# Kernel optimization log

Measured on AMD Instinct MI355X. Metric: run time of the kernel, lower is better.

The kernel has to match this reference:

```python
import jax, jax.numpy as jnp
import numpy as np

B, S, D_MODEL = 2, 2048, 1024
H, D = 16, 64
D_INNER = H * D
EPS = 1e-5


def setup_inputs() -> dict:
    key = jax.random.key(0)
    ks = jax.random.split(key, 10)
    sc = 0.02
    return {
        "x": jax.random.normal(ks[0], (B, S, D_MODEL), dtype=jnp.float32),
        "Wq": jax.random.normal(ks[1], (D_MODEL, D_INNER), dtype=jnp.float32) * sc,
        "Wk": jax.random.normal(ks[2], (D_MODEL, D_INNER), dtype=jnp.float32) * sc,
        "Wv": jax.random.normal(ks[3], (D_MODEL, D_INNER), dtype=jnp.float32) * sc,
        "Wg": jax.random.normal(ks[4], (D_MODEL, D_INNER), dtype=jnp.float32) * sc,
        "Wa": jax.random.normal(ks[5], (D_MODEL, H), dtype=jnp.float32) * sc,
        "ba": jax.random.normal(ks[6], (H,), dtype=jnp.float32) * sc,
        "Wo": jax.random.normal(ks[7], (D_INNER, D_MODEL), dtype=jnp.float32) * sc,
        "gn_w": jnp.ones((D_INNER,), dtype=jnp.float32),
        "gn_b": jnp.zeros((D_INNER,), dtype=jnp.float32),
    }


def reference(x, Wq, Wk, Wv, Wg, Wa, ba, Wo, gn_w, gn_b):
    b, s, _ = x.shape
    # projections -> [B,H,S,D]
    q = jax.nn.silu(jnp.einsum('bsm,md->bsd', x, Wq).reshape(b, s, H, D).transpose(0, 2, 1, 3))
    k = jax.nn.silu(jnp.einsum('bsm,md->bsd', x, Wk).reshape(b, s, H, D).transpose(0, 2, 1, 3))
    v = jnp.einsum('bsm,md->bsd', x, Wv).reshape(b, s, H, D).transpose(0, 2, 1, 3)

    # data-dependent log forget gate, per head: [B,H,S]
    log_alpha = -jax.nn.softplus(jnp.einsum('bsm,mh->bsh', x, Wa) + ba)
    cum = jnp.cumsum(log_alpha, axis=1).transpose(0, 2, 1)  # [B,H,S]

    # decay[b,h,i,j] = exp(cum[i] - cum[j]) for j <= i, else 0
    diff = cum[:, :, :, None] - cum[:, :, None, :]  # [B,H,S,S]
    causal = jnp.tril(jnp.ones((s, s), dtype=bool))
    decay = jnp.exp(jnp.where(causal, diff, -jnp.inf))

    attn = jnp.einsum('bhid,bhjd->bhij', q, k) * decay
    o = jnp.einsum('bhij,bhjd->bhid', attn, v)  # [B,H,S,D]
    o = o.transpose(0, 2, 1, 3)  # [B,S,H,D]

    # GroupNorm(H groups) over channels-within-group and spatial dim S
    mean = jnp.mean(o, axis=(1, 3), keepdims=True)          # per (b,h)
    var = jnp.var(o, axis=(1, 3), keepdims=True)
    o = (o - mean) / jnp.sqrt(var + EPS)
    o = o * gn_w.reshape(H, D) + gn_b.reshape(H, D)
    o = o.reshape(b, s, H * D)

    gate = jax.nn.sigmoid(jnp.einsum('bsm,md->bsd', x, Wg))
    return jnp.einsum('bsd,dm->bsm', o * gate, Wo)
```

## Files before the change

kernel.cpp:

```cpp
#include <hip/hip_runtime.h>
#include <math.h>
#include <stdint.h>

typedef __attribute__((ext_vector_type(4))) float f32x4;
typedef __attribute__((ext_vector_type(8))) short bf16x8;

constexpr int NB = 2;
constexpr int NS = 2048;
constexpr int NM = 1024;
constexpr int NH = 16;
constexpr int ND = 64;
constexpr int NDI = 1024;

__device__ __forceinline__ float bf2f(unsigned short u) {
  uint32_t x = ((uint32_t)u) << 16; float f; __builtin_memcpy(&f, &x, 4); return f;
}
__device__ __forceinline__ unsigned short f2bf(float f) {
  uint32_t x; __builtin_memcpy(&x, &f, 4);
  x += 0x7FFFu + ((x >> 16) & 1u);
  return (unsigned short)(x >> 16);
}

__global__ __launch_bounds__(256) void k_prep(const float* __restrict__ x,
    const float* __restrict__ w0, const float* __restrict__ w1,
    const float* __restrict__ w2, const float* __restrict__ w3,
    const float* __restrict__ w4, const float* __restrict__ Wa,
    unsigned short* __restrict__ xb,
    unsigned short* __restrict__ t0, unsigned short* __restrict__ t1,
    unsigned short* __restrict__ t2, unsigned short* __restrict__ t3,
    unsigned short* __restrict__ t4, unsigned short* __restrict__ wa_pad) {
  int bid = blockIdx.x;
  if (bid < 2048) {
    int i = bid * 256 + threadIdx.x;
    const float4* p = (const float4*)(x + (size_t)i * 8);
    float4 a = p[0], b = p[1];
    unsigned short r[8] = {f2bf(a.x), f2bf(a.y), f2bf(a.z), f2bf(a.w),
                           f2bf(b.x), f2bf(b.y), f2bf(b.z), f2bf(b.w)};
    *(uint4*)(xb + (size_t)i * 8) = *(const uint4*)r;
  } else if (bid < 7168) {
    __shared__ float tile[32][33];
    int w = bid - 2048;
    int z = w >> 10, within = w & 1023;
    const float* src = z == 0 ? w0 : z == 1 ? w1 : z == 2 ? w2 : z == 3 ? w3 : w4;
    unsigned short* dst = z == 0 ? t0 : z == 1 ? t1 : z == 2 ? t2 : z == 3 ? t3 : t4;
    int c0 = (within & 31) * 32, r0 = (within >> 5) * 32;
    int tx = threadIdx.x & 31, ty = threadIdx.x >> 5;
    #pragma unroll
    for (int i = 0; i < 4; i++)
      tile[ty + i * 8][tx] = src[(size_t)(r0 + ty + i * 8) * 1024 + c0 + tx];
    __syncthreads();
    #pragma unroll
    for (int i = 0; i < 4; i++)
      dst[(size_t)(c0 + ty + i * 8) * 1024 + r0 + tx] = f2bf(tile[tx][ty + i * 8]);
  } else {
    int idx = (bid - 7168) * 256 + threadIdx.x;
    int h = idx >> 10, k2 = idx & 1023;
    wa_pad[idx] = (h < 16) ? f2bf(Wa[k2 * 16 + h]) : (unsigned short)0;
  }
}

__global__ __launch_bounds__(256) void k_la_gemm(const unsigned short* __restrict__ xb,
    const unsigned short* __restrict__ wa_pad, float* __restrict__ la8) {
  __shared__ unsigned short As[128 * 32];
  __shared__ unsigned short Bs[128 * 32];
  int tid = threadIdx.x;
  int row0 = blockIdx.y * 128;
  int kbeg = blockIdx.x * 128;
  float* Cp = la8 + (size_t)blockIdx.x * (32 * 2048);
  int w = tid >> 6, l = tid & 63;
  int wr = w >> 1, wc = w & 1;
  int lr = l & 15, lk = l >> 4;
  f32x4 acc[4] = {};
  for (int k0 = kbeg; k0 < kbeg + 128; k0 += 32) {
    __syncthreads();
    #pragma unroll
    for (int i = 0; i < 2; i++) {
      int idx = tid + i * 256;
      int r = idx >> 2, c = idx & 3;
      int cs = c ^ ((r >> 1) & 3);
      const unsigned short* srcA = xb + (size_t)(row0 + r) * NM + k0 + cs * 8;
      const unsigned short* srcB = wa_pad + (size_t)r * NM + k0 + cs * 8;
      __builtin_amdgcn_global_load_lds(
          (const __attribute__((address_space(1))) void*)srcA,
          (__attribute__((address_space(3))) void*)((char*)As + (w * 64 + i * 256) * 16),
          16, 0, 0);
      __builtin_amdgcn_global_load_lds(
          (const __attribute__((address_space(1))) void*)srcB,
          (__attribute__((address_space(3))) void*)((char*)Bs + (w * 64 + i * 256) * 16),
          16, 0, 0);
    }
    __syncthreads();
    if (wc == 0) {
      bf16x8 b = *(const bf16x8*)&Bs[lr * 32 + (lk ^ ((lr >> 1) & 3)) * 8];
      #pragma unroll
      for (int m = 0; m < 4; m++) {
        int ra = wr * 64 + m * 16 + lr;
        bf16x8 a = *(const bf16x8*)&As[ra * 32 + (lk ^ ((ra >> 1) & 3)) * 8];
        acc[m] = __builtin_amdgcn_mfma_f32_16x16x32_bf16(a, b, acc[m], 0, 0, 0);
      }
    }
  }
  if (wc == 0) {
    #pragma unroll
    for (int m = 0; m < 4; m++) {
      #pragma unroll
      for (int j = 0; j < 4; j++) {
        int row = row0 + wr * 64 + m * 16 + lk * 4 + j;
        int bb = row >> 11, s = row & 2047;
        Cp[((size_t)(bb * 16 + lr)) * 2048 + s] = acc[m][j];
      }
    }
  }
}

__global__ __launch_bounds__(256) void k_cumsum(const float* __restrict__ la8,
    const float* __restrict__ ba, float* __restrict__ cum,
    float* __restrict__ psum, float* __restrict__ psq) {
  int g = blockIdx.x;
  int h = g & 15;
  if (threadIdx.x == 0) { psum[g] = 0.f; psq[g] = 0.f; }
  float bah = ba[h];
  const float* p0 = la8 + (size_t)g * NS;
  float* out = cum + (size_t)g * NS;
  __shared__ float part[256];
  float v[8]; float sum = 0.f;
  int base = threadIdx.x * 8;
  #pragma unroll
  for (int i = 0; i < 8; i++) {
    int s = base + i;
    float z = bah;
    #pragma unroll
    for (int sl = 0; sl < 8; sl++) z += p0[sl * 65536 + s];
    float sp = fmaxf(z, 0.f) + log1pf(expf(-fabsf(z)));
    v[i] = -sp; sum += v[i];
  }
  part[threadIdx.x] = sum;
  __syncthreads();
  for (int off = 1; off < 256; off <<= 1) {
    float add = (threadIdx.x >= off) ? part[threadIdx.x - off] : 0.f;
    __syncthreads();
    part[threadIdx.x] += add;
    __syncthreads();
  }
  float run = (threadIdx.x > 0) ? part[threadIdx.x - 1] : 0.f;
  #pragma unroll
  for (int i = 0; i < 8; i++) { run += v[i]; out[base + i] = run; }
}

__global__ __launch_bounds__(512, 2) void k_proj8(
    const unsigned short* __restrict__ A,
    const unsigned short* __restrict__ Wcat,
    unsigned short* __restrict__ q, unsigned short* __restrict__ k,
    unsigned short* __restrict__ v, unsigned short* __restrict__ g) {
  __shared__ unsigned short Ab[2][256 * 64];
  __shared__ unsigned short Bb[2][256 * 64];
  int tid = threadIdx.x;
  int bid = blockIdx.x;
  int wg = (bid & 7) * 32 + (bid >> 3);
  int bx = wg & 15, by = wg >> 4;
  int row0 = by * 256, col0 = bx * 256;
  int wid = tid >> 6, lane = tid & 63;
  int WR = wid >> 2, WC = wid & 3;
  int lr = lane & 15, lk = lane >> 4;

  auto stage = [&](int kt, int bi) {
    #pragma unroll
    for (int i = 0; i < 4; i++) {
      int idx = tid + i * 512;
      int r = idx >> 3, c = idx & 7;
      int cs = c ^ (r & 7);
      const unsigned short* srcA = A + (size_t)(row0 + r) * NM + kt * 64 + cs * 8;
      __builtin_amdgcn_global_load_lds(
          (const __attribute__((address_space(1))) void*)srcA,
          (__attribute__((address_space(3))) void*)((char*)&Ab[bi][0] + (wid * 64 + i * 512) * 16),
          16, 0, 0);
      const unsigned short* srcB = Wcat + (size_t)(col0 + r) * NM + kt * 64 + cs * 8;
      __builtin_amdgcn_global_load_lds(
          (const __attribute__((address_space(1))) void*)srcB,
          (__attribute__((address_space(3))) void*)((char*)&Bb[bi][0] + (wid * 64 + i * 512) * 16),
          16, 0, 0);
    }
  };

  stage(0, 0);
  stage(1, 1);

  f32x4 acc[8][4] = {};
  for (int kt = 0; kt < 16; ++kt) {
    int bi = kt & 1;
    if (kt < 15) asm volatile("s_waitcnt vmcnt(8)" ::: "memory");
    else         asm volatile("s_waitcnt vmcnt(0)" ::: "memory");
    __builtin_amdgcn_sched_barrier(0);
    __builtin_amdgcn_s_barrier();

    const char* Ap = (const char*)&Ab[bi][0];
    const char* Bp = (const char*)&Bb[bi][0];
    bf16x8 a0[8], b0[4], a1[8], b1[4];
    #pragma unroll
    for (int m = 0; m < 8; m++) {
      int r = WR * 128 + m * 16 + lr;
      a0[m] = *(const bf16x8*)(Ap + r * 128 + ((lk ^ (r & 7)) * 16));
    }
    #pragma unroll
    for (int n = 0; n < 4; n++) {
      int r = WC * 64 + n * 16 + lr;
      b0[n] = *(const bf16x8*)(Bp + r * 128 + ((lk ^ (r & 7)) * 16));
    }
    #pragma unroll
    for (int m = 0; m < 8; m++)
      #pragma unroll
      for (int n = 0; n < 4; n++)
        acc[m][n] = __builtin_amdgcn_mfma_f32_16x16x32_bf16(a0[m], b0[n], acc[m][n], 0, 0, 0);
    #pragma unroll
    for (int m = 0; m < 8; m++) {
      int r = WR * 128 + m * 16 + lr;
      a1[m] = *(const bf16x8*)(Ap + r * 128 + (((lk + 4) ^ (r & 7)) * 16));
    }
    #pragma unroll
    for (int n = 0; n < 4; n++) {
      int r = WC * 64 + n * 16 + lr;
      b1[n] = *(const bf16x8*)(Bp + r * 128 + (((lk + 4) ^ (r & 7)) * 16));
    }
    asm volatile("s_waitcnt lgkmcnt(0)" ::: "memory");
    __builtin_amdgcn_sched_barrier(0);
    __builtin_amdgcn_s_barrier();
    if (kt + 2 < 16) stage(kt + 2, bi);
    __builtin_amdgcn_s_setprio(1);
    #pragma unroll
    for (int m = 0; m < 8; m++)
      #pragma unroll
      for (int n = 0; n < 4; n++)
        acc[m][n] = __builtin_amdgcn_mfma_f32_16x16x32_bf16(a1[m], b1[n], acc[m][n], 0, 0, 0);
    __builtin_amdgcn_s_setprio(0);
  }

  #pragma unroll
  for (int m = 0; m < 8; m++) {
    #pragma unroll
    for (int n = 0; n < 4; n++) {
      int col = col0 + WC * 64 + n * 16 + lr;
      int zone = col >> 10;
      unsigned short* dst = zone == 0 ? q : zone == 1 ? k : zone == 2 ? v : g;
      int cb = col & 1023;
      #pragma unroll
      for (int j = 0; j < 4; j++) {
        int row = row0 + WR * 128 + m * 16 + lk * 4 + j;
        float val = acc[m][n][j];
        if (zone <= 1) val = val / (1.f + expf(-val));
        else if (zone == 3) val = 1.f / (1.f + expf(-val));
        dst[(size_t)row * 1024 + cb] = f2bf(val);
      }
    }
  }
}

__global__ __launch_bounds__(256) void k_out2(const unsigned short* __restrict__ A,
    const unsigned short* __restrict__ Bt, float* __restrict__ C) {
  __shared__ unsigned short As[2][128 * 64];
  __shared__ unsigned short Bs[2][128 * 64];
  int tid = threadIdx.x;
  int bid = blockIdx.x;
  int wg = (bid & 7) * 32 + (bid >> 3);
  int bx = wg & 7, by = wg >> 3;
  int row0 = by * 128, col0 = bx * 128;
  int w = tid >> 6, l = tid & 63;
  int wr = w >> 1, wc = w & 1;
  int lr = l & 15, lk = l >> 4;

  auto stage = [&](int t, int bi) {
    #pragma unroll
    for (int i = 0; i < 4; i++) {
      int idx = tid + i * 256;
      int r = idx >> 3, c = idx & 7;
      int cs = c ^ (r & 7);
      const unsigned short* srcA = A + (size_t)(row0 + r) * NM + t * 64 + cs * 8;
      __builtin_amdgcn_global_load_lds(
          (const __attribute__((address_space(1))) void*)srcA,
          (__attribute__((address_space(3))) void*)((char*)&As[bi][0] + idx * 16),
          16, 0, 0);
      const unsigned short* srcB = Bt + (size_t)(col0 + r) * NM + t * 64 + cs * 8;
      __builtin_amdgcn_global_load_lds(
          (const __attribute__((address_space(1))) void*)srcB,
          (__attribute__((address_space(3))) void*)((char*)&Bs[bi][0] + idx * 16),
          16, 0, 0);
    }
  };

  stage(0, 0);
  asm volatile("s_waitcnt vmcnt(0)" ::: "memory");
  __builtin_amdgcn_s_barrier();

  f32x4 acc[4][4] = {};
  int cur = 0;
  for (int t = 0; t < 16; ++t) {
    if (t < 15) stage(t + 1, cur ^ 1);
    const char* Ap = (const char*)&As[cur][0];
    const char* Bp = (const char*)&Bs[cur][0];
    bf16x8 a[4][2], b[4][2];
    #pragma unroll
    for (int m = 0; m < 4; m++) {
      int ra = wr * 64 + m * 16 + lr;
      #pragma unroll
      for (int kk = 0; kk < 2; kk++)
        a[m][kk] = *(const bf16x8*)(Ap + ra * 128 + (((kk * 4 + lk) ^ (ra & 7)) * 16));
    }
    #pragma unroll
    for (int n = 0; n < 4; n++) {
      int rb = wc * 64 + n * 16 + lr;
      #pragma unroll
      for (int kk = 0; kk < 2; kk++)
        b[n][kk] = *(const bf16x8*)(Bp + rb * 128 + (((kk * 4 + lk) ^ (rb & 7)) * 16));
    }
    __builtin_amdgcn_s_setprio(1);
    #pragma unroll
    for (int kk = 0; kk < 2; kk++)
      #pragma unroll
      for (int m = 0; m < 4; m++)
        #pragma unroll
        for (int n = 0; n < 4; n++)
          acc[m][n] = __builtin_amdgcn_mfma_f32_16x16x32_bf16(a[m][kk], b[n][kk], acc[m][n], 0, 0, 0);
    __builtin_amdgcn_s_setprio(0);
    asm volatile("s_waitcnt vmcnt(0)" ::: "memory");
    __builtin_amdgcn_s_barrier();
    cur ^= 1;
  }
  #pragma unroll
  for (int m = 0; m < 4; m++)
    #pragma unroll
    for (int n = 0; n < 4; n++)
      #pragma unroll
      for (int j = 0; j < 4; j++) {
        int row = row0 + wr * 64 + m * 16 + lk * 4 + j;
        int col = col0 + wc * 64 + n * 16 + lr;
        C[(size_t)row * NM + col] = acc[m][n][j];
      }
}

__global__ __launch_bounds__(256) void k_attn(const unsigned short* __restrict__ q,
    const unsigned short* __restrict__ kk, const unsigned short* __restrict__ vv,
    const float* __restrict__ cum, unsigned short* __restrict__ o,
    float* __restrict__ psum, float* __restrict__ psq) {
  int it = blockIdx.x, h = blockIdx.y, b = blockIdx.z;
  int i0 = it * 64;
  __shared__ unsigned short Qs[64 * 64];
  __shared__ unsigned short Ks[64 * 64];
  __shared__ unsigned short Ps[64 * 64];
  __shared__ unsigned short Vt[64 * 66];
  __shared__ float ci[64], cj[64];
  __shared__ int jlo_s;
  int tid = threadIdx.x;
  int w = tid >> 6, lane = tid & 63;
  int cl = lane & 15, hi = lane >> 4;
  const size_t hb = (size_t)b * NS * NDI + (size_t)h * ND;
  const float* cumh = cum + (size_t)(b * NH + h) * NS;

  #pragma unroll
  for (int lp = 0; lp < 2; lp++) {
    int idx = tid + lp * 256;
    int r = idx >> 3, cb = (idx & 7) * 16;
    uint4 t = *(const uint4*)(q + hb + (size_t)(i0 + r) * NDI + (cb >> 1));
    *(uint4*)((char*)Qs + r * 128 + (cb ^ ((r & 7) << 4))) = t;
  }
  if (tid < 64) ci[tid] = cumh[i0 + tid];
  if (tid < 64) {
    int jt = tid;
    bool ok = (jt <= it) && (cumh[i0] - cumh[jt * 64 + 63] >= -25.f);
    unsigned long long mask = __ballot(ok);
    if (tid == 0) jlo_s = (int)__builtin_ctzll(mask);
  }
  __syncthreads();
  int jlo = jlo_s;

  int arow = w * 16 + cl;
  int xr = (cl & 7) << 4;
  const char* Qb = (const char*)Qs + arow * 128;
  const char* Pb = (const char*)Ps + arow * 128;
  f32x4 acco[4] = {};

  for (int jt = jlo; jt <= it; jt++) {
    int j0 = jt * 64;
    __syncthreads();
    if (tid < 64) cj[tid] = cumh[j0 + tid];
    __syncthreads();
    #pragma unroll
    for (int lp = 0; lp < 2; lp++) {
      int idx = tid + lp * 256;
      int r = idx >> 3, cb = (idx & 7) * 16;
      uint4 t = *(const uint4*)(kk + hb + (size_t)(j0 + r) * NDI + (cb >> 1));
      *(uint4*)((char*)Ks + r * 128 + (cb ^ ((r & 7) << 4))) = t;
      uint4 tv = *(const uint4*)(vv + hb + (size_t)(j0 + r) * NDI + (cb >> 1));
      unsigned short us[8]; *(uint4*)us = tv;
      int c8 = (idx & 7) * 8;
      #pragma unroll
      for (int e = 0; e < 8; e++) Vt[(c8 + e) * 66 + r] = us[e];
    }
    __syncthreads();
    bf16x8 a0 = *(const bf16x8*)(Qb + ((hi * 16) ^ xr));
    bf16x8 a1 = *(const bf16x8*)(Qb + ((64 + hi * 16) ^ xr));
    f32x4 accs[4] = {};
    #pragma unroll
    for (int jtile = 0; jtile < 4; jtile++) {
      const char* Kb = (const char*)Ks + (jtile * 16 + cl) * 128;
      bf16x8 b0 = *(const bf16x8*)(Kb + ((hi * 16) ^ xr));
      bf16x8 b1 = *(const bf16x8*)(Kb + ((64 + hi * 16) ^ xr));
      accs[jtile] = __builtin_amdgcn_mfma_f32_16x16x32_bf16(a0, b0, accs[jtile], 0, 0, 0);
      accs[jtile] = __builtin_amdgcn_mfma_f32_16x16x32_bf16(a1, b1, accs[jtile], 0, 0, 0);
    }
    #pragma unroll
    for (int jtile = 0; jtile < 4; jtile++) {
      #pragma unroll
      for (int reg = 0; reg < 4; reg++) {
        int irl = w * 16 + hi * 4 + reg;
        int jl = jtile * 16 + cl;
        float dec = ((j0 + jl) <= (i0 + irl)) ? __expf(ci[irl] - cj[jl]) : 0.f;
        float pv = accs[jtile][reg] * dec;
        *(unsigned short*)((char*)Ps + irl * 128 + ((2 * jl) ^ ((irl & 7) << 4))) = f2bf(pv);
      }
    }
    __syncthreads();
    #pragma unroll
    for (int kk2 = 0; kk2 < 2; kk2++) {
      bf16x8 pa = *(const bf16x8*)(Pb + ((kk2 * 64 + hi * 16) ^ xr));
      #pragma unroll
      for (int dt = 0; dt < 4; dt++) {
        const unsigned int* vp = (const unsigned int*)(Vt + (dt * 16 + cl) * 66 + kk2 * 32 + hi * 8);
        uint4 tmp;
        tmp.x = vp[0]; tmp.y = vp[1]; tmp.z = vp[2]; tmp.w = vp[3];
        bf16x8 vb = *(const bf16x8*)&tmp;
        acco[dt] = __builtin_amdgcn_mfma_f32_16x16x32_bf16(pa, vb, acco[dt], 0, 0, 0);
      }
    }
  }
  #pragma unroll
  for (int dt = 0; dt < 4; dt++) {
    #pragma unroll
    for (int reg = 0; reg < 4; reg++) {
      int row = i0 + w * 16 + hi * 4 + reg;
      o[hb + (size_t)row * NDI + dt * 16 + cl] = f2bf(acco[dt][reg]);
    }
  }
  __syncthreads();
  float* ls = (float*)Ps;
  float* lq = ls + 256;
  float sm = 0.f, sq = 0.f;
  #pragma unroll
  for (int dt = 0; dt < 4; dt++)
    #pragma unroll
    for (int reg = 0; reg < 4; reg++) { float t2 = acco[dt][reg]; sm += t2; sq += t2 * t2; }
  ls[tid] = sm; lq[tid] = sq;
  __syncthreads();
  for (int off = 128; off > 0; off >>= 1) {
    if (tid < off) { ls[tid] += ls[tid + off]; lq[tid] += lq[tid + off]; }
    __syncthreads();
  }
  if (tid == 0) {
    atomicAdd(&psum[b * NH + h], ls[0]);
    atomicAdd(&psq[b * NH + h], lq[0]);
  }
}

__global__ __launch_bounds__(256) void k_gate(const unsigned short* __restrict__ o,
    const unsigned short* __restrict__ gsig, const float* __restrict__ psum,
    const float* __restrict__ psq, const float* __restrict__ gnw,
    const float* __restrict__ gnb, unsigned short* __restrict__ u) {
  int idx4 = blockIdx.x * 256 + threadIdx.x;
  size_t base = (size_t)idx4 * 4;
  int c = (int)(base & (NDI - 1));
  int row = (int)(base >> 10);
  int b = row >> 11;
  int h = c >> 6;
  int g = b * NH + h;
  float n = (float)(NS * ND);
  float mean = psum[g] / n;
  float var = psq[g] / n - mean * mean;
  float rstd = rsqrtf(var + 1e-5f);
  ushort4 ov = *(const ushort4*)(o + base);
  ushort4 gv = *(const ushort4*)(gsig + base);
  float4 w4 = *(const float4*)(gnw + c);
  float4 b4 = *(const float4*)(gnb + c);
  unsigned short r[4];
  r[0] = f2bf(((bf2f(ov.x) - mean) * rstd * w4.x + b4.x) * bf2f(gv.x));
  r[1] = f2bf(((bf2f(ov.y) - mean) * rstd * w4.y + b4.y) * bf2f(gv.y));
  r[2] = f2bf(((bf2f(ov.z) - mean) * rstd * w4.z + b4.z) * bf2f(gv.z));
  r[3] = f2bf(((bf2f(ov.w) - mean) * rstd * w4.w + b4.w) * bf2f(gv.w));
  *(ushort4*)(u + base) = *(const ushort4*)r;
}

extern "C" void kernel_launch(void* const* d_in, const int* in_sizes, int n_in,
                              void* d_out, int out_size, void* d_ws, size_t ws_size,
                              hipStream_t stream) {
  const float* x   = (const float*)d_in[0];
  const float* Wq  = (const float*)d_in[1];
  const float* Wk  = (const float*)d_in[2];
  const float* Wv  = (const float*)d_in[3];
  const float* Wg  = (const float*)d_in[4];
  const float* Wa  = (const float*)d_in[5];
  const float* ba  = (const float*)d_in[6];
  const float* Wo  = (const float*)d_in[7];
  const float* gnw = (const float*)d_in[8];
  const float* gnb = (const float*)d_in[9];
  float* out = (float*)d_out;

  const size_t NTOK = (size_t)NB * NS;
  char* p = (char*)d_ws;
  float* la8 = (float*)p;                 p += (size_t)8 * 32 * NS * 4;
  float* cum = (float*)p;                 p += (size_t)NB * NH * NS * 4;
  float* psum = (float*)p;                p += 32 * 4;
  float* psq  = (float*)p;                p += 32 * 4;
  p = (char*)(((uintptr_t)p + 255) & ~(uintptr_t)255);
  unsigned short* xb   = (unsigned short*)p; p += NTOK * NM * 2;
  unsigned short* Wcat = (unsigned short*)p; p += (size_t)4 * NM * NDI * 2;
  unsigned short* wto  = (unsigned short*)p; p += (size_t)NDI * NM * 2;
  unsigned short* wa_pad = (unsigned short*)p; p += (size_t)128 * NM * 2;
  unsigned short* q  = (unsigned short*)p;  p += NTOK * NDI * 2;
  unsigned short* k  = (unsigned short*)p;  p += NTOK * NDI * 2;
  unsigned short* v  = (unsigned short*)p;  p += NTOK * NDI * 2;
  unsigned short* g  = (unsigned short*)p;  p += NTOK * NDI * 2;
  unsigned short* u  = (unsigned short*)p;  p += NTOK * NDI * 2;
  unsigned short* o  = (unsigned short*)p;  p += NTOK * NDI * 2;

  unsigned short* wtq = Wcat;
  unsigned short* wtk = Wcat + (size_t)NM * NDI;
  unsigned short* wtv = Wcat + (size_t)2 * NM * NDI;
  unsigned short* wtg = Wcat + (size_t)3 * NM * NDI;

  k_prep    <<<dim3(7680), 256, 0, stream>>>(x, Wq, Wk, Wv, Wg, Wo, Wa,
                                             xb, wtq, wtk, wtv, wtg, wto, wa_pad);
  k_la_gemm <<<dim3(8, 32), 256, 0, stream>>>(xb, wa_pad, la8);
  k_cumsum  <<<dim3(NB * NH), 256, 0, stream>>>(la8, ba, cum, psum, psq);
  k_proj8   <<<dim3(256), 512, 0, stream>>>(xb, Wcat, q, k, v, g);
  k_attn    <<<dim3(32, NH, NB), 256, 0, stream>>>(q, k, v, cum, o, psum, psq);
  k_gate    <<<dim3(4096), 256, 0, stream>>>(o, g, psum, psq, gnw, gnb, u);
  k_out2    <<<dim3(256), 256, 0, stream>>>(u, wto, out);
}
```

Measured before the change: 121.6 us.

## Prefetch K/V tiles in attention, shrink out-proj tiles, use wave-shuffle reduction

The attention kernel now loads the next K/V tile from global memory into registers while the current tile is computed, and drops one barrier. The aim is to hide global load latency behind the MFMA work. The output GEMM uses 64x128 tiles over 512 blocks instead of 128x128 over 256, giving more blocks to fill the CUs at the cost of less reuse per tile. The GroupNorm statistic reduction replaces the shared-memory tree with wave shuffles, which cuts barriers.

Result: faster. 119.0 us, median of 2 (-2.2%).

```diff
diff --git a/kernel.cpp b/kernel.cpp
--- a/kernel.cpp
+++ b/kernel.cpp
@@ -256,20 +256,20 @@
 
 __global__ __launch_bounds__(256) void k_out2(const unsigned short* __restrict__ A,
     const unsigned short* __restrict__ Bt, float* __restrict__ C) {
-  __shared__ unsigned short As[2][128 * 64];
+  __shared__ unsigned short As[2][64 * 64];
   __shared__ unsigned short Bs[2][128 * 64];
   int tid = threadIdx.x;
   int bid = blockIdx.x;
-  int wg = (bid & 7) * 32 + (bid >> 3);
+  int wg = (bid & 7) * 64 + (bid >> 3);
   int bx = wg & 7, by = wg >> 3;
-  int row0 = by * 128, col0 = bx * 128;
+  int row0 = by * 64, col0 = bx * 128;
   int w = tid >> 6, l = tid & 63;
   int wr = w >> 1, wc = w & 1;
   int lr = l & 15, lk = l >> 4;
 
   auto stage = [&](int t, int bi) {
     #pragma unroll
-    for (int i = 0; i < 4; i++) {
+    for (int i = 0; i < 2; i++) {
       int idx = tid + i * 256;
       int r = idx >> 3, c = idx & 7;
       int cs = c ^ (r & 7);
@@ -278,6 +278,12 @@
           (const __attribute__((address_space(1))) void*)srcA,
           (__attribute__((address_space(3))) void*)((char*)&As[bi][0] + idx * 16),
           16, 0, 0);
+    }
+    #pragma unroll
+    for (int i = 0; i < 4; i++) {
+      int idx = tid + i * 256;
+      int r = idx >> 3, c = idx & 7;
+      int cs = c ^ (r & 7);
       const unsigned short* srcB = Bt + (size_t)(col0 + r) * NM + t * 64 + cs * 8;
       __builtin_amdgcn_global_load_lds(
           (const __attribute__((address_space(1))) void*)srcB,
@@ -290,16 +296,16 @@
   asm volatile("s_waitcnt vmcnt(0)" ::: "memory");
   __builtin_amdgcn_s_barrier();
 
-  f32x4 acc[4][4] = {};
+  f32x4 acc[2][4] = {};
   int cur = 0;
   for (int t = 0; t < 16; ++t) {
     if (t < 15) stage(t + 1, cur ^ 1);
     const char* Ap = (const char*)&As[cur][0];
     const char* Bp = (const char*)&Bs[cur][0];
-    bf16x8 a[4][2], b[4][2];
-    #pragma unroll
-    for (int m = 0; m < 4; m++) {
-      int ra = wr * 64 + m * 16 + lr;
+    bf16x8 a[2][2], b[4][2];
+    #pragma unroll
+    for (int m = 0; m < 2; m++) {
+      int ra = wr * 32 + m * 16 + lr;
       #pragma unroll
       for (int kk = 0; kk < 2; kk++)
         a[m][kk] = *(const bf16x8*)(Ap + ra * 128 + (((kk * 4 + lk) ^ (ra & 7)) * 16));
@@ -315,7 +321,7 @@
     #pragma unroll
     for (int kk = 0; kk < 2; kk++)
       #pragma unroll
-      for (int m = 0; m < 4; m++)
+      for (int m = 0; m < 2; m++)
         #pragma unroll
         for (int n = 0; n < 4; n++)
           acc[m][n] = __builtin_amdgcn_mfma_f32_16x16x32_bf16(a[m][kk], b[n][kk], acc[m][n], 0, 0, 0);
@@ -325,12 +331,12 @@
     cur ^= 1;
   }
   #pragma unroll
-  for (int m = 0; m < 4; m++)
+  for (int m = 0; m < 2; m++)
     #pragma unroll
     for (int n = 0; n < 4; n++)
       #pragma unroll
       for (int j = 0; j < 4; j++) {
-        int row = row0 + wr * 64 + m * 16 + lk * 4 + j;
+        int row = row0 + wr * 32 + m * 16 + lk * 4 + j;
         int col = col0 + wc * 64 + n * 16 + lr;
         C[(size_t)row * NM + col] = acc[m][n][j];
       }
@@ -377,23 +383,33 @@
   const char* Pb = (const char*)Ps + arow * 128;
   f32x4 acco[4] = {};
 
+  uint4 tK[2], tV[2];
+  auto gload = [&](int j0) {
+    #pragma unroll
+    for (int lp = 0; lp < 2; lp++) {
+      int idx = tid + lp * 256;
+      int r = idx >> 3, c8h = (idx & 7) * 8;
+      tK[lp] = *(const uint4*)(kk + hb + (size_t)(j0 + r) * NDI + c8h);
+      tV[lp] = *(const uint4*)(vv + hb + (size_t)(j0 + r) * NDI + c8h);
+    }
+  };
+  if (jlo <= it) gload(jlo * 64);
+
   for (int jt = jlo; jt <= it; jt++) {
     int j0 = jt * 64;
     __syncthreads();
     if (tid < 64) cj[tid] = cumh[j0 + tid];
-    __syncthreads();
     #pragma unroll
     for (int lp = 0; lp < 2; lp++) {
       int idx = tid + lp * 256;
       int r = idx >> 3, cb = (idx & 7) * 16;
-      uint4 t = *(const uint4*)(kk + hb + (size_t)(j0 + r) * NDI + (cb >> 1));
-      *(uint4*)((char*)Ks + r * 128 + (cb ^ ((r & 7) << 4))) = t;
-      uint4 tv = *(const uint4*)(vv + hb + (size_t)(j0 + r) * NDI + (cb >> 1));
-      unsigned short us[8]; *(uint4*)us = tv;
+      *(uint4*)((char*)Ks + r * 128 + (cb ^ ((r & 7) << 4))) = tK[lp];
+      unsigned short us[8]; *(uint4*)us = tV[lp];
       int c8 = (idx & 7) * 8;
       #pragma unroll
       for (int e = 0; e < 8; e++) Vt[(c8 + e) * 66 + r] = us[e];
     }
+    if (jt + 1 <= it) gload(j0 + 64);
     __syncthreads();
     bf16x8 a0 = *(const bf16x8*)(Qb + ((hi * 16) ^ xr));
     bf16x8 a1 = *(const bf16x8*)(Qb + ((64 + hi * 16) ^ xr));
@@ -439,23 +455,26 @@
       o[hb + (size_t)row * NDI + dt * 16 + cl] = f2bf(acco[dt][reg]);
     }
   }
+  float sm = 0.f, sq = 0.f;
+  #pragma unroll
+  for (int dt = 0; dt < 4; dt++)
+    #pragma unroll
+    for (int reg = 0; reg < 4; reg++) { float t2 = acco[dt][reg]; sm += t2; sq += t2 * t2; }
+  #pragma unroll
+  for (int off = 32; off > 0; off >>= 1) {
+    sm += __shfl_down(sm, off, 64);
+    sq += __shfl_down(sq, off, 64);
+  }
   __syncthreads();
-  float* ls = (float*)Ps;
-  float* lq = ls + 256;
-  float sm = 0.f, sq = 0.f;
-  #pragma unroll
-  for (int dt = 0; dt < 4; dt++)
-    #pragma unroll
-    for (int reg = 0; reg < 4; reg++) { float t2 = acco[dt][reg]; sm += t2; sq += t2 * t2; }
-  ls[tid] = sm; lq[tid] = sq;
+  float* ws2 = (float*)Ps;
+  if (lane == 0) { ws2[w * 2] = sm; ws2[w * 2 + 1] = sq; }
   __syncthreads();
-  for (int off = 128; off > 0; off >>= 1) {
-    if (tid < off) { ls[tid] += ls[tid + off]; lq[tid] += lq[tid + off]; }
-    __syncthreads();
-  }
   if (tid == 0) {
-    atomicAdd(&psum[b * NH + h], ls[0]);
-    atomicAdd(&psq[b * NH + h], lq[0]);
+    float S = 0.f, Q2 = 0.f;
+    #pragma unroll
+    for (int i = 0; i < 4; i++) { S += ws2[i * 2]; Q2 += ws2[i * 2 + 1]; }
+    atomicAdd(&psum[b * NH + h], S);
+    atomicAdd(&psq[b * NH + h], Q2);
   }
 }
 
@@ -531,5 +550,5 @@
   k_proj8   <<<dim3(256), 512, 0, stream>>>(xb, Wcat, q, k, v, g);
   k_attn    <<<dim3(32, NH, NB), 256, 0, stream>>>(q, k, v, cum, o, psum, psq);
   k_gate    <<<dim3(4096), 256, 0, stream>>>(o, g, psum, psq, gnw, gnb, u);
-  k_out2    <<<dim3(256), 256, 0, stream>>>(u, wto, out);
-}
+  k_out2    <<<dim3(512), 256, 0, stream>>>(u, wto, out);
+}
```
